# Performance work log

Measured on AMD Instinct MI355X. Metric: run time of the kernel, lower is better.

Reference implementation:

```python
import jax, jax.numpy as jnp
import numpy as np

ATOM_VOC = 128
PAD = 0

def setup_inputs() -> dict:
    key = jax.random.key(0)
    ks = jax.random.split(key, 12)
    b, l, d_model, nhead, apo = 8, 256, 512, 16, 128
    atoms = jax.random.randint(ks[0], (b, l), 0, ATOM_VOC)
    chirals = jax.random.randint(ks[1], (b, l), 0, 4)
    coordinates = jax.random.normal(ks[2], (b, l, 3), dtype=jnp.float32)
    bonds = jax.random.randint(ks[3], (b, l, l), 0, 32)
    atype_emb = jax.random.normal(ks[4], (ATOM_VOC, d_model), jnp.float32).at[PAD].set(0.0)
    chiral_emb = jax.random.normal(ks[5], (4, d_model), jnp.float32).at[PAD].set(0.0)
    apair_w_tab = jax.random.normal(ks[6], (ATOM_VOC * ATOM_VOC, apo), jnp.float32)
    apair_b_tab = jax.random.normal(ks[7], (ATOM_VOC * ATOM_VOC, apo), jnp.float32)
    means = jnp.zeros((apo,), jnp.float32)
    stds = jnp.ones((apo,), jnp.float32)
    bond_emb = jax.random.normal(ks[8], (32, nhead), jnp.float32).at[PAD].set(0.0)
    lin_w = jax.random.normal(ks[9], (apo, nhead), jnp.float32) / np.sqrt(apo)
    lin_b = jax.random.normal(ks[10], (nhead,), jnp.float32)
    return dict(atoms=atoms, chirals=chirals, coordinates=coordinates, bonds=bonds,
                atype_emb=atype_emb, chiral_emb=chiral_emb, apair_w_tab=apair_w_tab,
                apair_b_tab=apair_b_tab, means=means, stds=stds, bond_emb=bond_emb,
                lin_w=lin_w, lin_b=lin_b)

def _safe_dist(coordinates):
    # pairwise distances [b,l,l]; safe-sqrt so grad at 0 distance is 0 (diagonal)
    diff = coordinates[:, None, :, :] - coordinates[:, :, None, :]
    s = jnp.sum(diff * diff, axis=-1)
    return jnp.where(s > 0, jnp.sqrt(jnp.where(s > 0, s, 1.0)), 0.0)

def reference(atoms, chirals, coordinates, bonds, atype_emb, chiral_emb,
              apair_w_tab, apair_b_tab, means, stds, bond_emb, lin_w, lin_b):
    # atoms_emb: [l, b, d_model]
    atoms_emb = (atype_emb[atoms] + chiral_emb[chirals]).transpose(1, 0, 2)
    dist = _safe_dist(coordinates)                      # [b,l,l]
    pair_idx = atoms[:, None, :] * ATOM_VOC + atoms[:, :, None]  # [b,l,l]
    ap = apair_w_tab[pair_idx] * dist[..., None] + apair_b_tab[pair_idx]  # [b,l,l,apo]
    std = jnp.abs(stds) + 1e-5
    gauss = jnp.exp(-0.5 * ((ap - means) / std) ** 2) / (np.sqrt(2.0 * np.pi) * std)
    apairs = jnp.einsum('bijk,kh->bijh', gauss, lin_w) + lin_b + bond_emb[bonds]
    pad_mask = (atoms == PAD)[:, None, :, None]         # mask over key/column dim
    apairs = jnp.where(pad_mask, -jnp.inf, apairs)
    return atoms_emb, apairs.transpose(0, 3, 1, 2)      # [b,nhead,l,l]
```

## Files before the change

kernel.cpp:

```cpp
#include <hip/hip_runtime.h>
#include <hip/hip_fp16.h>
#include <math.h>
#include <stdint.h>

#define B 8
#define L 256
#define DM 512
#define NH 16
#define APO 128
#define VOC 128
#define EMB (L * B * DM)

typedef __attribute__((ext_vector_type(4))) _Float16 half4v;
typedef __attribute__((ext_vector_type(4))) float float4v;

#define WSB_BOFF   1024
#define PACK_BOFF  8192
#define PACK_BYTES (128 * 128 * 256)
#define WS_NEED    ((size_t)PACK_BOFF + (size_t)PACK_BYTES)

__device__ __forceinline__ void g2lds16(const void* g, void* l) {
    __builtin_amdgcn_global_load_lds(
        (const __attribute__((address_space(1))) unsigned int*)g,
        (__attribute__((address_space(3))) unsigned int*)l, 16, 0, 0);
}

__global__ __launch_bounds__(256) void prep_kernel(const float* __restrict__ means,
                                                   const float* __restrict__ stds,
                                                   const float* __restrict__ lin_w,
                                                   float* __restrict__ ws) {
    int t = threadIdx.x;
    const float gscale = 0.3989422804014327f;
    unsigned short* wsB = (unsigned short*)((char*)ws + WSB_BOFF);
    for (int idx = t; idx < 8 * 64 * 4; idx += 256) {
        int p = idx >> 8;
        int lane = (idx >> 2) & 63;
        int e = idx & 3;
        int k = p * 16 + ((lane >> 4) << 2) + e;
        int h = lane & 15;
        float sigma = fabsf(stds[k]) + 1e-5f;
        float v = lin_w[k * NH + h] * (gscale / sigma);
        __half hv = __float2half(v);
        wsB[idx] = *reinterpret_cast<unsigned short*>(&hv);
    }
}

__global__ __launch_bounds__(256) void pack_kernel(const float* __restrict__ wtab,
                                                   const float* __restrict__ btab,
                                                   const float* __restrict__ means,
                                                   const float* __restrict__ stds,
                                                   float* __restrict__ ws) {
    const float beta = sqrtf(0.5f * 1.4426950408889634f);
    int idx = blockIdx.x * 256 + threadIdx.x;
    int r = idx >> 5;
    int a_i = r >> 7, a_j = r & 127;
    int u = idx & 31;
    int k0 = u * 4;
    size_t src = ((size_t)a_j * VOC + a_i) * APO + k0;
    const float4* w4p = (const float4*)(wtab + src);
    const float4* b4p = (const float4*)(btab + src);
    float4 w4 = *w4p, b4 = *b4p;
    float wq[4], bq[4];
    #pragma unroll
    for (int e = 0; e < 4; ++e) {
        int k = k0 + e;
        float sigma = fabsf(stds[k]) + 1e-5f;
        float ia = beta / sigma;
        float wv = ((const float*)&w4)[e] * ia;
        float bv = (((const float*)&b4)[e] - means[k]) * ia;
        wq[e] = wv; bq[e] = bv;
    }
    int wdw = 0, bdw = 0;
    wdw = __builtin_amdgcn_cvt_pk_fp8_f32(wq[0], wq[1], wdw, 0);
    wdw = __builtin_amdgcn_cvt_pk_fp8_f32(wq[2], wq[3], wdw, 1);
    bdw = __builtin_amdgcn_cvt_pk_fp8_f32(bq[0], bq[1], bdw, 0);
    bdw = __builtin_amdgcn_cvt_pk_fp8_f32(bq[2], bq[3], bdw, 1);
    int pu = u ^ (a_j & 31);
    uint2 o; o.x = (unsigned)wdw; o.y = (unsigned)bdw;
    *(uint2*)((char*)ws + PACK_BOFF + (size_t)r * 256 + (size_t)pu * 8) = o;
}

__global__ __launch_bounds__(256, 5) void pair_fused(const int* __restrict__ atoms,
                                                     const int* __restrict__ chirals,
                                                     const float* __restrict__ coords,
                                                     const int* __restrict__ bonds,
                                                     const float* __restrict__ atype,
                                                     const float* __restrict__ chiral,
                                                     const float* __restrict__ bond_emb,
                                                     const float* __restrict__ lin_b,
                                                     const float* __restrict__ ws,
                                                     float* __restrict__ out) {
    __shared__ __align__(16) char stage[32 * 1024];

    int t = threadIdx.x;
    int bid = blockIdx.x;
    int bi = bid >> 8, i = bid & 255;
    int w = t >> 6, l = t & 63;

    if (t < 128) {
        int a = atoms[bi * L + i];
        int c = chirals[bi * L + i];
        const float4* va = (const float4*)(atype + (size_t)a * DM);
        const float4* vc = (const float4*)(chiral + (size_t)c * DM);
        float4 x = va[t], y = vc[t];
        x.x += y.x; x.y += y.y; x.z += y.z; x.w += y.w;
        ((float4*)(out + ((size_t)i * B + bi) * DM))[t] = x;
    }

    int a_i = atoms[bi * L + i];
    int av = atoms[bi * L + t];

    float cix = coords[((size_t)bi * L + i) * 3 + 0];
    float ciy = coords[((size_t)bi * L + i) * 3 + 1];
    float ciz = coords[((size_t)bi * L + i) * 3 + 2];
    float cjx = coords[((size_t)bi * L + t) * 3 + 0];
    float cjy = coords[((size_t)bi * L + t) * 3 + 1];
    float cjz = coords[((size_t)bi * L + t) * 3 + 2];
    float dx = cjx - cix, dy = cjy - ciy, dz = cjz - ciz;
    float s2 = dx * dx + dy * dy + dz * dz;
    float d = (s2 > 0.0f) ? sqrtf(s2) : 0.0f;
    int dbits = __float_as_int(d);

    half4v bfrag[8];
    {
        const uint2* wb = (const uint2*)((const char*)ws + WSB_BOFF);
        #pragma unroll
        for (int p = 0; p < 8; ++p) {
            uint2 r = wb[p * 64 + l];
            bfrag[p] = *reinterpret_cast<half4v*>(&r);
        }
    }

    int m = l >> 4;
    float dval[4];
    int base[4], ax[4];
    #pragma unroll
    for (int q = 0; q < 4; ++q) {
        int idx4 = (q * 16 + (l & 15)) * 4;
        int a = __builtin_amdgcn_ds_bpermute(idx4, av);
        dval[q] = __int_as_float(__builtin_amdgcn_ds_bpermute(idx4, dbits));
        base[q] = a * 256;
        ax[q] = a & 31;
    }

    float4v acc[4];
    #pragma unroll
    for (int q = 0; q < 4; ++q) { float4v z = {0, 0, 0, 0}; acc[q] = z; }

    const char* pkbi = (const char*)ws + PACK_BOFF + (size_t)a_i * 32768;

    asm volatile("s_waitcnt vmcnt(0)" ::: "memory");
    __builtin_amdgcn_sched_barrier(0);
    #pragma unroll
    for (int it = 0; it < 8; ++it) {
        size_t off = (size_t)(w * 32 + it * 4) * 256 + (size_t)l * 16;
        g2lds16(pkbi + off, stage + off);
    }
    asm volatile("s_waitcnt vmcnt(0)" ::: "memory");
    __syncthreads();

    #pragma unroll
    for (int rr = 0; rr < 8; ++rr) {
        #pragma unroll
        for (int q = 0; q < 4; ++q) {
            int un = (rr * 4 + m) ^ ax[q];
            uint2 wb = *(const uint2*)(stage + base[q] + (un << 3));
            auto w01 = __builtin_amdgcn_cvt_pk_f32_fp8((int)wb.x, 0);
            auto w23 = __builtin_amdgcn_cvt_pk_f32_fp8((int)wb.x, 1);
            auto b01 = __builtin_amdgcn_cvt_pk_f32_fp8((int)wb.y, 0);
            auto b23 = __builtin_amdgcn_cvt_pk_f32_fp8((int)wb.y, 1);
            float dq = dval[q];
            float t0 = fmaf(w01[0], dq, b01[0]);
            float t1 = fmaf(w01[1], dq, b01[1]);
            float t2 = fmaf(w23[0], dq, b23[0]);
            float t3 = fmaf(w23[1], dq, b23[1]);
            float g0 = __builtin_amdgcn_exp2f(-(t0 * t0));
            float g1 = __builtin_amdgcn_exp2f(-(t1 * t1));
            float g2 = __builtin_amdgcn_exp2f(-(t2 * t2));
            float g3 = __builtin_amdgcn_exp2f(-(t3 * t3));
            auto lo = __builtin_amdgcn_cvt_pkrtz(g0, g1);
            auto hi = __builtin_amdgcn_cvt_pkrtz(g2, g3);
            uint2 au;
            au.x = *reinterpret_cast<unsigned*>(&lo);
            au.y = *reinterpret_cast<unsigned*>(&hi);
            half4v af = *reinterpret_cast<half4v*>(&au);
            acc[q] = __builtin_amdgcn_mfma_f32_16x16x16f16(af, bfrag[rr],
                                                           acc[q], 0, 0, 0);
        }
    }

    asm volatile("s_waitcnt lgkmcnt(0)" ::: "memory");
    __syncthreads();

    int a_j = atoms[bi * L + t];
    int bvd = bonds[(((size_t)bi * L) + i) * L + t];
    float beh[NH];
    {
        const float4* ber = (const float4*)(bond_emb + (size_t)bvd * NH);
        #pragma unroll
        for (int u = 0; u < 4; ++u) {
            float4 v4 = ber[u];
            beh[u * 4 + 0] = v4.x; beh[u * 4 + 1] = v4.y;
            beh[u * 4 + 2] = v4.z; beh[u * 4 + 3] = v4.w;
        }
    }
    float* cbuf = (float*)(stage + (size_t)w * 4352);
    {
        int h = l & 15, jg = l >> 4;
        #pragma unroll
        for (int q = 0; q < 4; ++q)
            *(float4v*)(cbuf + h * 68 + q * 16 + jg * 4) = acc[q];
    }
    asm volatile("s_waitcnt lgkmcnt(0)" ::: "memory");
    __builtin_amdgcn_sched_barrier(0);

    size_t obase = (((size_t)bi * NH) * L + i) * L + t;
    float ninf = __uint_as_float(0xff7f0000u);
    bool pad = (a_j == 0);
    #pragma unroll
    for (int h = 0; h < NH; ++h) {
        float v = cbuf[h * 68 + l] + lin_b[h] + beh[h];
        out[(size_t)EMB + obase + (size_t)h * L * L] = pad ? ninf : v;
    }
}

extern "C" void kernel_launch(void* const* d_in, const int* in_sizes, int n_in,
                              void* d_out, int out_size, void* d_ws, size_t ws_size,
                              hipStream_t stream) {
    const int*   atoms    = (const int*)d_in[0];
    const int*   chirals  = (const int*)d_in[1];
    const float* coords   = (const float*)d_in[2];
    const int*   bonds    = (const int*)d_in[3];
    const float* atype    = (const float*)d_in[4];
    const float* chiral   = (const float*)d_in[5];
    const float* wtab     = (const float*)d_in[6];
    const float* btab     = (const float*)d_in[7];
    const float* means    = (const float*)d_in[8];
    const float* stds     = (const float*)d_in[9];
    const float* bond_emb = (const float*)d_in[10];
    const float* lin_w    = (const float*)d_in[11];
    const float* lin_b    = (const float*)d_in[12];
    float* out = (float*)d_out;
    float* ws  = (float*)d_ws;

    prep_kernel<<<1, 256, 0, stream>>>(means, stds, lin_w, ws);
    pack_kernel<<<2048, 256, 0, stream>>>(wtab, btab, means, stds, ws);
    pair_fused<<<B * L, 256, 0, stream>>>(atoms, chirals, coords, bonds,
                                          atype, chiral, bond_emb, lin_b, ws, out);
}
```

Measured before the change: 36.81 us.

## Switch to 16x16x32 f16 MFMA with 16-byte packed fp8 table and merged prep

Repacks the fp8 pair table into 16-byte chunks of 8 k-values, so each lane does one 128-bit LDS read per MFMA step. The 16x16x16 f16 MFMA is replaced with the gfx950 16x16x32 f16 MFMA, which halves the MFMA count. The prep kernel is folded into block 0 of the pack kernel, removing one launch, and the pack grid is halved because each thread now handles 8 values. The atom-embedding store is moved after the LDS staging barrier so it overlaps with the compute loop, at the cost of wider registers per iteration.

```diff
diff --git a/kernel.cpp b/kernel.cpp
--- a/kernel.cpp
+++ b/kernel.cpp
@@ -11,11 +11,11 @@
 #define VOC 128
 #define EMB (L * B * DM)
 
-typedef __attribute__((ext_vector_type(4))) _Float16 half4v;
+typedef __attribute__((ext_vector_type(8))) _Float16 half8v;
 typedef __attribute__((ext_vector_type(4))) float float4v;
 
 #define WSB_BOFF   1024
-#define PACK_BOFF  8192
+#define PACK_BOFF  16384
 #define PACK_BYTES (128 * 128 * 256)
 #define WS_NEED    ((size_t)PACK_BOFF + (size_t)PACK_BYTES)
 
@@ -25,59 +25,65 @@
         (__attribute__((address_space(3))) unsigned int*)l, 16, 0, 0);
 }
 
-__global__ __launch_bounds__(256) void prep_kernel(const float* __restrict__ means,
-                                                   const float* __restrict__ stds,
-                                                   const float* __restrict__ lin_w,
-                                                   float* __restrict__ ws) {
-    int t = threadIdx.x;
-    const float gscale = 0.3989422804014327f;
-    unsigned short* wsB = (unsigned short*)((char*)ws + WSB_BOFF);
-    for (int idx = t; idx < 8 * 64 * 4; idx += 256) {
-        int p = idx >> 8;
-        int lane = (idx >> 2) & 63;
-        int e = idx & 3;
-        int k = p * 16 + ((lane >> 4) << 2) + e;
-        int h = lane & 15;
-        float sigma = fabsf(stds[k]) + 1e-5f;
-        float v = lin_w[k * NH + h] * (gscale / sigma);
-        __half hv = __float2half(v);
-        wsB[idx] = *reinterpret_cast<unsigned short*>(&hv);
-    }
-}
-
 __global__ __launch_bounds__(256) void pack_kernel(const float* __restrict__ wtab,
                                                    const float* __restrict__ btab,
                                                    const float* __restrict__ means,
                                                    const float* __restrict__ stds,
+                                                   const float* __restrict__ lin_w,
                                                    float* __restrict__ ws) {
     const float beta = sqrtf(0.5f * 1.4426950408889634f);
-    int idx = blockIdx.x * 256 + threadIdx.x;
-    int r = idx >> 5;
+    const float gscale = 0.3989422804014327f;
+    int t = threadIdx.x;
+
+    if (blockIdx.x == 0) {
+        unsigned short* wsB = (unsigned short*)((char*)ws + WSB_BOFF);
+        for (int idx = t; idx < 4 * 64 * 8; idx += 256) {
+            int p = idx >> 9;
+            int lane = (idx >> 3) & 63;
+            int e = idx & 7;
+            int k = p * 32 + ((lane >> 4) << 3) + e;
+            int h = lane & 15;
+            float sigma = fabsf(stds[k]) + 1e-5f;
+            float v = lin_w[k * NH + h] * (gscale / sigma);
+            __half hv = __float2half(v);
+            wsB[idx] = *reinterpret_cast<unsigned short*>(&hv);
+        }
+    }
+
+    int idx = blockIdx.x * 256 + t;
+    int r = idx >> 4;
     int a_i = r >> 7, a_j = r & 127;
-    int u = idx & 31;
-    int k0 = u * 4;
+    int U = idx & 15;
+    int k0 = U * 8;
     size_t src = ((size_t)a_j * VOC + a_i) * APO + k0;
     const float4* w4p = (const float4*)(wtab + src);
     const float4* b4p = (const float4*)(btab + src);
-    float4 w4 = *w4p, b4 = *b4p;
-    float wq[4], bq[4];
-    #pragma unroll
-    for (int e = 0; e < 4; ++e) {
+    float4 w0 = w4p[0], w1 = w4p[1], b0 = b4p[0], b1 = b4p[1];
+    float wq[8], bq[8];
+    #pragma unroll
+    for (int e = 0; e < 8; ++e) {
         int k = k0 + e;
         float sigma = fabsf(stds[k]) + 1e-5f;
         float ia = beta / sigma;
-        float wv = ((const float*)&w4)[e] * ia;
-        float bv = (((const float*)&b4)[e] - means[k]) * ia;
-        wq[e] = wv; bq[e] = bv;
-    }
-    int wdw = 0, bdw = 0;
-    wdw = __builtin_amdgcn_cvt_pk_fp8_f32(wq[0], wq[1], wdw, 0);
-    wdw = __builtin_amdgcn_cvt_pk_fp8_f32(wq[2], wq[3], wdw, 1);
-    bdw = __builtin_amdgcn_cvt_pk_fp8_f32(bq[0], bq[1], bdw, 0);
-    bdw = __builtin_amdgcn_cvt_pk_fp8_f32(bq[2], bq[3], bdw, 1);
-    int pu = u ^ (a_j & 31);
-    uint2 o; o.x = (unsigned)wdw; o.y = (unsigned)bdw;
-    *(uint2*)((char*)ws + PACK_BOFF + (size_t)r * 256 + (size_t)pu * 8) = o;
+        float wvv = ((e < 4) ? ((const float*)&w0)[e] : ((const float*)&w1)[e - 4]) * ia;
+        float bvv = (((e < 4) ? ((const float*)&b0)[e] : ((const float*)&b1)[e - 4])
+                     - means[k]) * ia;
+        wq[e] = wvv; bq[e] = bvv;
+    }
+    int wlo = 0, whi = 0, blo = 0, bhi = 0;
+    wlo = __builtin_amdgcn_cvt_pk_fp8_f32(wq[0], wq[1], wlo, 0);
+    wlo = __builtin_amdgcn_cvt_pk_fp8_f32(wq[2], wq[3], wlo, 1);
+    whi = __builtin_amdgcn_cvt_pk_fp8_f32(wq[4], wq[5], whi, 0);
+    whi = __builtin_amdgcn_cvt_pk_fp8_f32(wq[6], wq[7], whi, 1);
+    blo = __builtin_amdgcn_cvt_pk_fp8_f32(bq[0], bq[1], blo, 0);
+    blo = __builtin_amdgcn_cvt_pk_fp8_f32(bq[2], bq[3], blo, 1);
+    bhi = __builtin_amdgcn_cvt_pk_fp8_f32(bq[4], bq[5], bhi, 0);
+    bhi = __builtin_amdgcn_cvt_pk_fp8_f32(bq[6], bq[7], bhi, 1);
+    int pu = U ^ (a_j & 15);
+    uint4 o;
+    o.x = (unsigned)wlo; o.y = (unsigned)whi;
+    o.z = (unsigned)blo; o.w = (unsigned)bhi;
+    *(uint4*)((char*)ws + PACK_BOFF + (size_t)r * 256 + (size_t)pu * 16) = o;
 }
 
 __global__ __launch_bounds__(256, 5) void pair_fused(const int* __restrict__ atoms,
@@ -97,16 +103,6 @@
     int bi = bid >> 8, i = bid & 255;
     int w = t >> 6, l = t & 63;
 
-    if (t < 128) {
-        int a = atoms[bi * L + i];
-        int c = chirals[bi * L + i];
-        const float4* va = (const float4*)(atype + (size_t)a * DM);
-        const float4* vc = (const float4*)(chiral + (size_t)c * DM);
-        float4 x = va[t], y = vc[t];
-        x.x += y.x; x.y += y.y; x.z += y.z; x.w += y.w;
-        ((float4*)(out + ((size_t)i * B + bi) * DM))[t] = x;
-    }
-
     int a_i = atoms[bi * L + i];
     int av = atoms[bi * L + t];
 
@@ -121,13 +117,13 @@
     float d = (s2 > 0.0f) ? sqrtf(s2) : 0.0f;
     int dbits = __float_as_int(d);
 
-    half4v bfrag[8];
+    half8v bfrag[4];
     {
-        const uint2* wb = (const uint2*)((const char*)ws + WSB_BOFF);
-        #pragma unroll
-        for (int p = 0; p < 8; ++p) {
-            uint2 r = wb[p * 64 + l];
-            bfrag[p] = *reinterpret_cast<half4v*>(&r);
+        const uint4* wb = (const uint4*)((const char*)ws + WSB_BOFF);
+        #pragma unroll
+        for (int p = 0; p < 4; ++p) {
+            uint4 r = wb[p * 64 + l];
+            bfrag[p] = *reinterpret_cast<half8v*>(&r);
         }
     }
 
@@ -140,7 +136,7 @@
         int a = __builtin_amdgcn_ds_bpermute(idx4, av);
         dval[q] = __int_as_float(__builtin_amdgcn_ds_bpermute(idx4, dbits));
         base[q] = a * 256;
-        ax[q] = a & 31;
+        ax[q] = a & 15;
     }
 
     float4v acc[4];
@@ -159,33 +155,59 @@
     asm volatile("s_waitcnt vmcnt(0)" ::: "memory");
     __syncthreads();
 
-    #pragma unroll
-    for (int rr = 0; rr < 8; ++rr) {
+    if (t < 128) {
+        int a = atoms[bi * L + i];
+        int c = chirals[bi * L + i];
+        const float4* va = (const float4*)(atype + (size_t)a * DM);
+        const float4* vc = (const float4*)(chiral + (size_t)c * DM);
+        float4 x = va[t], y = vc[t];
+        x.x += y.x; x.y += y.y; x.z += y.z; x.w += y.w;
+        ((float4*)(out + ((size_t)i * B + bi) * DM))[t] = x;
+    }
+
+    #pragma unroll
+    for (int rr = 0; rr < 4; ++rr) {
         #pragma unroll
         for (int q = 0; q < 4; ++q) {
             int un = (rr * 4 + m) ^ ax[q];
-            uint2 wb = *(const uint2*)(stage + base[q] + (un << 3));
-            auto w01 = __builtin_amdgcn_cvt_pk_f32_fp8((int)wb.x, 0);
-            auto w23 = __builtin_amdgcn_cvt_pk_f32_fp8((int)wb.x, 1);
-            auto b01 = __builtin_amdgcn_cvt_pk_f32_fp8((int)wb.y, 0);
-            auto b23 = __builtin_amdgcn_cvt_pk_f32_fp8((int)wb.y, 1);
+            uint4 u = *(const uint4*)(stage + base[q] + (un << 4));
+            auto w01 = __builtin_amdgcn_cvt_pk_f32_fp8((int)u.x, 0);
+            auto w23 = __builtin_amdgcn_cvt_pk_f32_fp8((int)u.x, 1);
+            auto w45 = __builtin_amdgcn_cvt_pk_f32_fp8((int)u.y, 0);
+            auto w67 = __builtin_amdgcn_cvt_pk_f32_fp8((int)u.y, 1);
+            auto b01 = __builtin_amdgcn_cvt_pk_f32_fp8((int)u.z, 0);
+            auto b23 = __builtin_amdgcn_cvt_pk_f32_fp8((int)u.z, 1);
+            auto b45 = __builtin_amdgcn_cvt_pk_f32_fp8((int)u.w, 0);
+            auto b67 = __builtin_amdgcn_cvt_pk_f32_fp8((int)u.w, 1);
             float dq = dval[q];
             float t0 = fmaf(w01[0], dq, b01[0]);
             float t1 = fmaf(w01[1], dq, b01[1]);
             float t2 = fmaf(w23[0], dq, b23[0]);
             float t3 = fmaf(w23[1], dq, b23[1]);
+            float t4 = fmaf(w45[0], dq, b45[0]);
+            float t5 = fmaf(w45[1], dq, b45[1]);
+            float t6 = fmaf(w67[0], dq, b67[0]);
+            float t7 = fmaf(w67[1], dq, b67[1]);
             float g0 = __builtin_amdgcn_exp2f(-(t0 * t0));
             float g1 = __builtin_amdgcn_exp2f(-(t1 * t1));
             float g2 = __builtin_amdgcn_exp2f(-(t2 * t2));
             float g3 = __builtin_amdgcn_exp2f(-(t3 * t3));
-            auto lo = __builtin_amdgcn_cvt_pkrtz(g0, g1);
-            auto hi = __builtin_amdgcn_cvt_pkrtz(g2, g3);
-            uint2 au;
-            au.x = *reinterpret_cast<unsigned*>(&lo);
-            au.y = *reinterpret_cast<unsigned*>(&hi);
-            half4v af = *reinterpret_cast<half4v*>(&au);
-            acc[q] = __builtin_amdgcn_mfma_f32_16x16x16f16(af, bfrag[rr],
-                                                           acc[q], 0, 0, 0);
+            float g4 = __builtin_amdgcn_exp2f(-(t4 * t4));
+            float g5 = __builtin_amdgcn_exp2f(-(t5 * t5));
+            float g6 = __builtin_amdgcn_exp2f(-(t6 * t6));
+            float g7 = __builtin_amdgcn_exp2f(-(t7 * t7));
+            auto p0 = __builtin_amdgcn_cvt_pkrtz(g0, g1);
+            auto p1 = __builtin_amdgcn_cvt_pkrtz(g2, g3);
+            auto p2 = __builtin_amdgcn_cvt_pkrtz(g4, g5);
+            auto p3 = __builtin_amdgcn_cvt_pkrtz(g6, g7);
+            uint4 au;
+            au.x = *reinterpret_cast<unsigned*>(&p0);
+            au.y = *reinterpret_cast<unsigned*>(&p1);
+            au.z = *reinterpret_cast<unsigned*>(&p2);
+            au.w = *reinterpret_cast<unsigned*>(&p3);
+            half8v af = *reinterpret_cast<half8v*>(&au);
+            acc[q] = __builtin_amdgcn_mfma_f32_16x16x32_f16(af, bfrag[rr],
+                                                            acc[q], 0, 0, 0);
         }
     }
 
@@ -243,8 +265,7 @@
     float* out = (float*)d_out;
     float* ws  = (float*)d_ws;
 
-    prep_kernel<<<1, 256, 0, stream>>>(means, stds, lin_w, ws);
-    pack_kernel<<<2048, 256, 0, stream>>>(wtab, btab, means, stds, ws);
+    pack_kernel<<<1024, 256, 0, stream>>>(wtab, btab, means, stds, lin_w, ws);
     pair_fused<<<B * L, 256, 0, stream>>>(atoms, chirals, coords, bonds,
                                           atype, chiral, bond_emb, lin_b, ws, out);
 }
```

New measurement: 33.02 us. 1.11x faster.
